# Performance work log

Measured on AMD Instinct MI355X. Metric: run time of the kernel, lower is better.

Reference implementation:

```python
import jax, jax.numpy as jnp
import numpy as np

B, C_IN, C_OUT, A, H, W = 32, 256, 512, 256, 64, 64


def setup_inputs() -> dict:
    key = jax.random.key(0)
    ks = jax.random.split(key, 8)
    s = 0.02
    return {
        "x": jax.random.normal(ks[0], (B, C_IN, H, W), dtype=jnp.float32),
        "g": jax.random.normal(ks[1], (B, C_OUT), dtype=jnp.float32),
        "Wg": jax.random.normal(ks[2], (A, C_OUT), dtype=jnp.float32) * s,
        "bg": jnp.full((A,), 0.1, dtype=jnp.float32),
        "Wx": jax.random.normal(ks[3], (A, C_IN), dtype=jnp.float32) * s,
        "bx": jnp.full((A,), 0.1, dtype=jnp.float32),
        "Wf": jax.random.normal(ks[4], (1, A), dtype=jnp.float32) * s,
        "bf": jnp.full((1,), 0.1, dtype=jnp.float32),
    }


def reference(x, g, Wg, bg, Wx, bx, Wf, bf):
    b, c, h, w = x.shape
    gg = g @ Wg.T + bg                                  # [B, A]
    xf = x.reshape(b, c, h * w)                          # [B, C, HW]
    # Linear_x applied per spatial position (batched instead of python loop)
    nx = jnp.einsum('bcn,ac->bna', xf, Wx) + bx          # [B, HW, A]
    nx = jax.nn.relu(gg[:, None, :] + nx)                # [B, HW, A]
    att = jnp.einsum('bna,a->bn', nx, Wf[0]) + bf[0]     # [B, HW]
    # min-subtract, sum-divide normalization
    att = att - jnp.min(att, axis=1, keepdims=True)
    att = att / jnp.sum(att, axis=1, keepdims=True)
    out = jnp.einsum('bcn,bn->bc', xf, att)              # weighted pooling [B, C]
    return out, att.reshape(b, h, w)
```

## Files before the change

kernel.cpp:

```cpp
#include <hip/hip_runtime.h>
#include <stdint.h>

#define B_   32
#define CIN  256
#define COUT 512
#define A_   256
#define HW_  4096
#define NT   64
#define TILES 8

typedef short  short8  __attribute__((ext_vector_type(8)));
typedef float  float4_ __attribute__((ext_vector_type(4)));

__device__ __forceinline__ unsigned f2bf(float f) {
    unsigned u = __float_as_uint(f);
    u += 0x7FFFu + ((u >> 16) & 1u);
    return u >> 16;
}
__device__ __forceinline__ float bf2f(unsigned h) {
    return __uint_as_float(h << 16);
}

__global__ __launch_bounds__(256) void prep_kernel(
    const float* __restrict__ g, const float* __restrict__ Wg,
    const float* __restrict__ bg, const float* __restrict__ Wx,
    const float* __restrict__ bx,
    uint4* __restrict__ WxR, float* __restrict__ ggbx,
    float* __restrict__ P, float* __restrict__ T)
{
    int t = threadIdx.x;
    if (blockIdx.x >= 32) {
        int e = (blockIdx.x - 32) * 256 + t;
        int lane = e & 63, ai = (e >> 6) & 3, kk = (e >> 8) & 7, w = e >> 11;
        int a  = w * 64 + ai * 16 + (lane & 15);
        int kb = kk * 32 + (lane >> 4) * 8;
        const float4* s = (const float4*)(Wx + (size_t)a * 256 + kb);
        float4 u0 = s[0], u1 = s[1];
        uint4 pk;
        pk.x = f2bf(u0.x) | (f2bf(u0.y) << 16);
        pk.y = f2bf(u0.z) | (f2bf(u0.w) << 16);
        pk.z = f2bf(u1.x) | (f2bf(u1.y) << 16);
        pk.w = f2bf(u1.z) | (f2bf(u1.w) << 16);
        WxR[e] = pk;
        return;
    }
    int b = blockIdx.x;
    int i = b * 256 + t;
    P[i] = 0.f; T[i] = 0.f;

    __shared__ float gl[COUT];
    gl[t]       = g[b * COUT + t];
    gl[t + 256] = g[b * COUT + 256 + t];
    __syncthreads();

    float acc0 = bg[t] + bx[t], acc1 = 0.f;
    const float4* wr = (const float4*)(Wg + (size_t)t * COUT);
    #pragma unroll 8
    for (int co = 0; co < COUT / 4; co += 2) {
        float4 wv0 = wr[co],     gv0 = *(const float4*)&gl[co * 4];
        float4 wv1 = wr[co + 1], gv1 = *(const float4*)&gl[co * 4 + 4];
        acc0 += wv0.x * gv0.x + wv0.y * gv0.y + wv0.z * gv0.z + wv0.w * gv0.w;
        acc1 += wv1.x * gv1.x + wv1.y * gv1.y + wv1.z * gv1.z + wv1.w * gv1.w;
    }
    ggbx[b * 256 + t] = acc0 + acc1;
}

__global__ __launch_bounds__(512)
__attribute__((amdgpu_waves_per_eu(2, 2)))
void attn_main(
    const float* __restrict__ x, const char* __restrict__ WxR,
    const float* __restrict__ ggbx, const float* __restrict__ Wf,
    const float* __restrict__ bfs,
    float* __restrict__ P, float* __restrict__ T, float* __restrict__ raw)
{
    __shared__ unsigned int xT[2][NT * 128];
    __shared__ float att_part[8][NT];
    __shared__ float raw_l[NT];

    int bid = blockIdx.x;
    int b = bid >> 3, tg = bid & 7;
    int t = threadIdx.x, w = t >> 6, lane = t & 63;
    int quad = lane >> 4, l15 = lane & 15;

    const float* xb = x + (size_t)b * CIN * HW_ + tg * (TILES * NT);

    short8 bfp[16];
    {
        const char* wsl = WxR + (w >> 1) * 32768 + (w & 1) * 2048 + lane * 16;
        #pragma unroll
        for (int kk = 0; kk < 8; kk++) {
            bfp[kk * 2]     = *(const short8*)(wsl + kk * 4096);
            bfp[kk * 2 + 1] = *(const short8*)(wsl + kk * 4096 + 1024);
        }
    }

    float4_ ga4[2], wf4[2];
    #pragma unroll
    for (int ai = 0; ai < 2; ai++) {
        int a0 = w * 32 + ai * 16 + quad * 4;
        ga4[ai] = *(const float4_*)&ggbx[b * 256 + a0];
        wf4[ai] = *(const float4_*)&Wf[a0];
    }

    int n4 = l15 * 4;
    int cb = w * 32 + quad * 8;
    int qc = cb >> 3;
    const float* xrow = xb + (size_t)cb * HW_ + n4;

    float4_ v[8];
    #pragma unroll
    for (int j = 0; j < 8; j++)
        v[j] = *(const float4_*)(xrow + (size_t)j * HW_);
    #pragma unroll
    for (int r = 0; r < 4; r++) {
        uint4 pk;
        pk.x = f2bf(v[0][r]) | (f2bf(v[1][r]) << 16);
        pk.y = f2bf(v[2][r]) | (f2bf(v[3][r]) << 16);
        pk.z = f2bf(v[4][r]) | (f2bf(v[5][r]) << 16);
        pk.w = f2bf(v[6][r]) | (f2bf(v[7][r]) << 16);
        int n = n4 + r;
        *(uint4*)&xT[0][n * 128 + ((qc ^ (n & 31)) << 2)] = pk;
    }

    float pp[4] = {0.f, 0.f, 0.f, 0.f};
    float tt[4] = {0.f, 0.f, 0.f, 0.f};
    int qpt   = (t & 63) >> 1;
    int half  = (t & 1) * 8;
    int nbase = w * 8;

    __syncthreads();

    #pragma unroll 1
    for (int it = 0; it < TILES; it++) {
        const unsigned int* xl = xT[it & 1];
        unsigned int* xw = xT[(it + 1) & 1];

        if (it < TILES - 1) {
            const float* xn = xrow + (it + 1) * NT;
            #pragma unroll
            for (int j = 0; j < 8; j++)
                v[j] = *(const float4_*)(xn + (size_t)j * HW_);
        }
        __builtin_amdgcn_sched_barrier(0);

        float4_ acc[4][2];
        #pragma unroll
        for (int mi = 0; mi < 4; mi++) {
            acc[mi][0] = (float4_){0.f, 0.f, 0.f, 0.f};
            acc[mi][1] = (float4_){0.f, 0.f, 0.f, 0.f};
        }
        short8 afA[4], afB[4];
        auto LDA = [&](short8* af, int k0) {
            int qk = (k0 >> 3) + quad;
            #pragma unroll
            for (int mi = 0; mi < 4; mi++) {
                int n = mi * 16 + l15;
                af[mi] = *(const short8*)&xl[n * 128 + ((qk ^ (n & 31)) << 2)];
            }
        };
        auto MM = [&](short8* af, int ks) {
            #pragma unroll
            for (int mi = 0; mi < 4; mi++) {
                acc[mi][0] = __builtin_amdgcn_mfma_f32_16x16x32_bf16(
                    bfp[ks * 2],     af[mi], acc[mi][0], 0, 0, 0);
                acc[mi][1] = __builtin_amdgcn_mfma_f32_16x16x32_bf16(
                    bfp[ks * 2 + 1], af[mi], acc[mi][1], 0, 0, 0);
            }
        };

        LDA(afA, 0);   LDA(afB, 32);
        MM(afA, 0);    LDA(afA, 64);
        MM(afB, 1);    LDA(afB, 96);
        MM(afA, 2);    LDA(afA, 128);
        MM(afB, 3);    LDA(afB, 160);
        MM(afA, 4);    LDA(afA, 192);
        MM(afB, 5);    LDA(afB, 224);
        MM(afA, 6);
        MM(afB, 7);

        #pragma unroll
        for (int mi = 0; mi < 4; mi++) {
            float p = 0.f;
            #pragma unroll
            for (int ai = 0; ai < 2; ai++) {
                #pragma unroll
                for (int r = 0; r < 4; r++) {
                    float vv = fmaxf(acc[mi][ai][r] + ga4[ai][r], 0.f);
                    p = fmaf(vv, wf4[ai][r], p);
                }
            }
            p += __shfl_xor(p, 16, 64);
            p += __shfl_xor(p, 32, 64);
            if (quad == 0) att_part[w][mi * 16 + l15] = p;
        }
        __syncthreads();

        if (t < NT) {
            float rv = att_part[0][t] + att_part[1][t] + att_part[2][t] + att_part[3][t]
                     + att_part[4][t] + att_part[5][t] + att_part[6][t] + att_part[7][t]
                     + bfs[0];
            raw[b * HW_ + (tg * TILES + it) * NT + t] = rv;
            raw_l[t] = rv;
        }
        __syncthreads();

        #pragma unroll
        for (int i = 0; i < 8; i++) {
            int n = nbase + i;
            uint2 u = *(const uint2*)((const char*)xl + n * 512 + ((qpt ^ (n & 31)) << 4) + half);
            float rv = raw_l[n];
            float x0 = bf2f(u.x & 0xFFFFu), x1 = bf2f(u.x >> 16);
            float x2 = bf2f(u.y & 0xFFFFu), x3 = bf2f(u.y >> 16);
            pp[0] = fmaf(x0, rv, pp[0]); tt[0] += x0;
            pp[1] = fmaf(x1, rv, pp[1]); tt[1] += x1;
            pp[2] = fmaf(x2, rv, pp[2]); tt[2] += x2;
            pp[3] = fmaf(x3, rv, pp[3]); tt[3] += x3;
        }

        if (it < TILES - 1) {
            #pragma unroll
            for (int r = 0; r < 4; r++) {
                uint4 pk;
                pk.x = f2bf(v[0][r]) | (f2bf(v[1][r]) << 16);
                pk.y = f2bf(v[2][r]) | (f2bf(v[3][r]) << 16);
                pk.z = f2bf(v[4][r]) | (f2bf(v[5][r]) << 16);
                pk.w = f2bf(v[6][r]) | (f2bf(v[7][r]) << 16);
                int n = n4 + r;
                *(uint4*)&xw[n * 128 + ((qc ^ (n & 31)) << 2)] = pk;
            }
        }
        __syncthreads();
    }

    {
        float* red = (float*)xT;
        float4_* pr = (float4_*)(red + w * 512);
        float4_* tr = (float4_*)(red + w * 512 + 256);
        pr[lane] = (float4_){pp[0], pp[1], pp[2], pp[3]};
        tr[lane] = (float4_){tt[0], tt[1], tt[2], tt[3]};
        __syncthreads();
        int sel = t >> 8, cc = t & 255;
        float s = 0.f;
        #pragma unroll
        for (int g = 0; g < 8; g++)
            s += red[g * 512 + sel * 256 + cc];
        atomicAdd((sel ? T : P) + b * 256 + cc, s);
    }
}

__global__ __launch_bounds__(256) void finalize_kernel(
    const float* __restrict__ raw, const float* __restrict__ P,
    const float* __restrict__ T, float* __restrict__ out)
{
    int b = blockIdx.x, t = threadIdx.x;
    const float* r = raw + (size_t)b * HW_;
    float v[16];
    float mn = 3.4e38f, sm = 0.f;
    #pragma unroll
    for (int i = 0; i < 16; i++) {
        v[i] = r[t + 256 * i];
        mn = fminf(mn, v[i]);
        sm += v[i];
    }
    #pragma unroll
    for (int off = 1; off < 64; off <<= 1) {
        mn = fminf(mn, __shfl_xor(mn, off, 64));
        sm += __shfl_xor(sm, off, 64);
    }
    __shared__ float smn[4], ssm[4];
    int w = t >> 6;
    if ((t & 63) == 0) { smn[w] = mn; ssm[w] = sm; }
    __syncthreads();
    mn = fminf(fminf(smn[0], smn[1]), fminf(smn[2], smn[3]));
    sm = (ssm[0] + ssm[1]) + (ssm[2] + ssm[3]);
    float S = sm - 4096.f * mn;
    float inv = 1.f / S;

    float* att = out + B_ * CIN + (size_t)b * HW_;
    #pragma unroll
    for (int i = 0; i < 16; i++) att[t + 256 * i] = (v[i] - mn) * inv;

    int ic = b * 256 + t;
    out[ic] = (P[ic] - mn * T[ic]) * inv;
}

extern "C" void kernel_launch(void* const* d_in, const int* in_sizes, int n_in,
                              void* d_out, int out_size, void* d_ws, size_t ws_size,
                              hipStream_t stream)
{
    const float* x   = (const float*)d_in[0];
    const float* g   = (const float*)d_in[1];
    const float* Wg  = (const float*)d_in[2];
    const float* bg  = (const float*)d_in[3];
    const float* Wx  = (const float*)d_in[4];
    const float* bx  = (const float*)d_in[5];
    const float* Wf  = (const float*)d_in[6];
    const float* bf  = (const float*)d_in[7];
    float* out = (float*)d_out;

    char* wsb = (char*)d_ws;
    uint4* WxR  = (uint4*)wsb;
    float* ggbx = (float*)(wsb + 131072);
    float* P    = ggbx + 8192;
    float* T    = P + 8192;
    float* raw  = T + 8192;

    prep_kernel<<<64, 256, 0, stream>>>(g, Wg, bg, Wx, bx, WxR, ggbx, P, T);
    attn_main<<<256, 512, 0, stream>>>(x, (const char*)WxR, ggbx, Wf, bf, P, T, raw);
    finalize_kernel<<<32, 256, 0, stream>>>(raw, P, T, out);
}
```

Baseline: 231.6 us.

## Split attention block across 16 waves with 16 attention channels each

```diff
diff --git a/kernel.cpp b/kernel.cpp
--- a/kernel.cpp
+++ b/kernel.cpp
@@ -65,8 +65,8 @@
     ggbx[b * 256 + t] = acc0 + acc1;
 }
 
-__global__ __launch_bounds__(512)
-__attribute__((amdgpu_waves_per_eu(2, 2)))
+__global__ __launch_bounds__(1024)
+__attribute__((amdgpu_waves_per_eu(4, 4)))
 void attn_main(
     const float* __restrict__ x, const char* __restrict__ WxR,
     const float* __restrict__ ggbx, const float* __restrict__ Wf,
@@ -74,7 +74,7 @@
     float* __restrict__ P, float* __restrict__ T, float* __restrict__ raw)
 {
     __shared__ unsigned int xT[2][NT * 128];
-    __shared__ float att_part[8][NT];
+    __shared__ float att_part[16][NT];
     __shared__ float raw_l[NT];
 
     int bid = blockIdx.x;
@@ -84,49 +84,45 @@
 
     const float* xb = x + (size_t)b * CIN * HW_ + tg * (TILES * NT);
 
-    short8 bfp[16];
+    short8 bfp[8];
     {
-        const char* wsl = WxR + (w >> 1) * 32768 + (w & 1) * 2048 + lane * 16;
-        #pragma unroll
-        for (int kk = 0; kk < 8; kk++) {
-            bfp[kk * 2]     = *(const short8*)(wsl + kk * 4096);
-            bfp[kk * 2 + 1] = *(const short8*)(wsl + kk * 4096 + 1024);
-        }
-    }
-
-    float4_ ga4[2], wf4[2];
-    #pragma unroll
-    for (int ai = 0; ai < 2; ai++) {
-        int a0 = w * 32 + ai * 16 + quad * 4;
-        ga4[ai] = *(const float4_*)&ggbx[b * 256 + a0];
-        wf4[ai] = *(const float4_*)&Wf[a0];
+        const char* wsl = WxR + (w >> 2) * 32768 + (w & 3) * 1024 + lane * 16;
+        #pragma unroll
+        for (int kk = 0; kk < 8; kk++)
+            bfp[kk] = *(const short8*)(wsl + kk * 4096);
+    }
+
+    float4_ ga4, wf4;
+    {
+        int a0 = w * 16 + quad * 4;
+        ga4 = *(const float4_*)&ggbx[b * 256 + a0];
+        wf4 = *(const float4_*)&Wf[a0];
     }
 
     int n4 = l15 * 4;
-    int cb = w * 32 + quad * 8;
+    int cb = w * 16 + quad * 4;
     int qc = cb >> 3;
+    int hb = (cb & 4) << 1;
     const float* xrow = xb + (size_t)cb * HW_ + n4;
 
-    float4_ v[8];
-    #pragma unroll
-    for (int j = 0; j < 8; j++)
+    float4_ v[4];
+    #pragma unroll
+    for (int j = 0; j < 4; j++)
         v[j] = *(const float4_*)(xrow + (size_t)j * HW_);
     #pragma unroll
     for (int r = 0; r < 4; r++) {
-        uint4 pk;
+        uint2 pk;
         pk.x = f2bf(v[0][r]) | (f2bf(v[1][r]) << 16);
         pk.y = f2bf(v[2][r]) | (f2bf(v[3][r]) << 16);
-        pk.z = f2bf(v[4][r]) | (f2bf(v[5][r]) << 16);
-        pk.w = f2bf(v[6][r]) | (f2bf(v[7][r]) << 16);
         int n = n4 + r;
-        *(uint4*)&xT[0][n * 128 + ((qc ^ (n & 31)) << 2)] = pk;
+        *(uint2*)((char*)xT[0] + n * 512 + ((qc ^ (n & 31)) << 4) + hb) = pk;
     }
 
     float pp[4] = {0.f, 0.f, 0.f, 0.f};
     float tt[4] = {0.f, 0.f, 0.f, 0.f};
     int qpt   = (t & 63) >> 1;
     int half  = (t & 1) * 8;
-    int nbase = w * 8;
+    int nbase = w * 4;
 
     __syncthreads();
 
@@ -138,56 +134,38 @@
         if (it < TILES - 1) {
             const float* xn = xrow + (it + 1) * NT;
             #pragma unroll
-            for (int j = 0; j < 8; j++)
+            for (int j = 0; j < 4; j++)
                 v[j] = *(const float4_*)(xn + (size_t)j * HW_);
         }
         __builtin_amdgcn_sched_barrier(0);
 
-        float4_ acc[4][2];
-        #pragma unroll
-        for (int mi = 0; mi < 4; mi++) {
-            acc[mi][0] = (float4_){0.f, 0.f, 0.f, 0.f};
-            acc[mi][1] = (float4_){0.f, 0.f, 0.f, 0.f};
-        }
-        short8 afA[4], afB[4];
-        auto LDA = [&](short8* af, int k0) {
-            int qk = (k0 >> 3) + quad;
+        float4_ acc[4];
+        #pragma unroll
+        for (int mi = 0; mi < 4; mi++)
+            acc[mi] = (float4_){0.f, 0.f, 0.f, 0.f};
+
+        #pragma unroll
+        for (int ks = 0; ks < 8; ks++) {
+            int qk = ks * 4 + quad;
+            short8 af[4];
             #pragma unroll
             for (int mi = 0; mi < 4; mi++) {
                 int n = mi * 16 + l15;
                 af[mi] = *(const short8*)&xl[n * 128 + ((qk ^ (n & 31)) << 2)];
             }
-        };
-        auto MM = [&](short8* af, int ks) {
-            #pragma unroll
-            for (int mi = 0; mi < 4; mi++) {
-                acc[mi][0] = __builtin_amdgcn_mfma_f32_16x16x32_bf16(
-                    bfp[ks * 2],     af[mi], acc[mi][0], 0, 0, 0);
-                acc[mi][1] = __builtin_amdgcn_mfma_f32_16x16x32_bf16(
-                    bfp[ks * 2 + 1], af[mi], acc[mi][1], 0, 0, 0);
-            }
-        };
-
-        LDA(afA, 0);   LDA(afB, 32);
-        MM(afA, 0);    LDA(afA, 64);
-        MM(afB, 1);    LDA(afB, 96);
-        MM(afA, 2);    LDA(afA, 128);
-        MM(afB, 3);    LDA(afB, 160);
-        MM(afA, 4);    LDA(afA, 192);
-        MM(afB, 5);    LDA(afB, 224);
-        MM(afA, 6);
-        MM(afB, 7);
+            #pragma unroll
+            for (int mi = 0; mi < 4; mi++)
+                acc[mi] = __builtin_amdgcn_mfma_f32_16x16x32_bf16(
+                    bfp[ks], af[mi], acc[mi], 0, 0, 0);
+        }
 
         #pragma unroll
         for (int mi = 0; mi < 4; mi++) {
             float p = 0.f;
             #pragma unroll
-            for (int ai = 0; ai < 2; ai++) {
-                #pragma unroll
-                for (int r = 0; r < 4; r++) {
-                    float vv = fmaxf(acc[mi][ai][r] + ga4[ai][r], 0.f);
-                    p = fmaf(vv, wf4[ai][r], p);
-                }
+            for (int r = 0; r < 4; r++) {
+                float vv = fmaxf(acc[mi][r] + ga4[r], 0.f);
+                p = fmaf(vv, wf4[r], p);
             }
             p += __shfl_xor(p, 16, 64);
             p += __shfl_xor(p, 32, 64);
@@ -196,16 +174,16 @@
         __syncthreads();
 
         if (t < NT) {
-            float rv = att_part[0][t] + att_part[1][t] + att_part[2][t] + att_part[3][t]
-                     + att_part[4][t] + att_part[5][t] + att_part[6][t] + att_part[7][t]
-                     + bfs[0];
+            float rv = bfs[0];
+            #pragma unroll
+            for (int g = 0; g < 16; g++) rv += att_part[g][t];
             raw[b * HW_ + (tg * TILES + it) * NT + t] = rv;
             raw_l[t] = rv;
         }
         __syncthreads();
 
         #pragma unroll
-        for (int i = 0; i < 8; i++) {
+        for (int i = 0; i < 4; i++) {
             int n = nbase + i;
             uint2 u = *(const uint2*)((const char*)xl + n * 512 + ((qpt ^ (n & 31)) << 4) + half);
             float rv = raw_l[n];
@@ -220,13 +198,11 @@
         if (it < TILES - 1) {
             #pragma unroll
             for (int r = 0; r < 4; r++) {
-                uint4 pk;
+                uint2 pk;
                 pk.x = f2bf(v[0][r]) | (f2bf(v[1][r]) << 16);
                 pk.y = f2bf(v[2][r]) | (f2bf(v[3][r]) << 16);
-                pk.z = f2bf(v[4][r]) | (f2bf(v[5][r]) << 16);
-                pk.w = f2bf(v[6][r]) | (f2bf(v[7][r]) << 16);
                 int n = n4 + r;
-                *(uint4*)&xw[n * 128 + ((qc ^ (n & 31)) << 2)] = pk;
+                *(uint2*)((char*)xw + n * 512 + ((qc ^ (n & 31)) << 4) + hb) = pk;
             }
         }
         __syncthreads();
@@ -239,12 +215,14 @@
         pr[lane] = (float4_){pp[0], pp[1], pp[2], pp[3]};
         tr[lane] = (float4_){tt[0], tt[1], tt[2], tt[3]};
         __syncthreads();
-        int sel = t >> 8, cc = t & 255;
-        float s = 0.f;
-        #pragma unroll
-        for (int g = 0; g < 8; g++)
-            s += red[g * 512 + sel * 256 + cc];
-        atomicAdd((sel ? T : P) + b * 256 + cc, s);
+        if (t < 512) {
+            int sel = t >> 8, cc = t & 255;
+            float s = 0.f;
+            #pragma unroll
+            for (int g = 0; g < 16; g++)
+                s += red[g * 512 + sel * 256 + cc];
+            atomicAdd((sel ? T : P) + b * 256 + cc, s);
+        }
     }
 }
 
@@ -306,6 +284,6 @@
     float* raw  = T + 8192;
 
     prep_kernel<<<64, 256, 0, stream>>>(g, Wg, bg, Wx, bx, WxR, ggbx, P, T);
-    attn_main<<<256, 512, 0, stream>>>(x, (const char*)WxR, ggbx, Wf, bf, P, T, raw);
+    attn_main<<<256, 1024, 0, stream>>>(x, (const char*)WxR, ggbx, Wf, bf, P, T, raw);
     finalize_kernel<<<32, 256, 0, stream>>>(raw, P, T, out);
 }
```

New measurement: 255.4 us. +10.3%, slower.
